# Kernel optimization log

Hardware: AMD Instinct MI355X
Metric: run time of the kernel (lower is better)

The kernel has to match this reference:

```python
import jax, jax.numpy as jnp
import numpy as np

DIM = 1536
NUM_HEADS = 24
HEAD_DIM = DIM // NUM_HEADS
SCALE = HEAD_DIM ** -0.5
B, NX, NC = 2, 2048, 256


def setup_inputs() -> dict:
    key = jax.random.key(0)
    ks = jax.random.split(key, 12)
    s = 0.02
    return {
        "x": jax.random.normal(ks[0], (B, NX, DIM), jnp.float32),
        "c": jax.random.normal(ks[1], (B, NC, DIM), jnp.float32),
        "Wqkv_x": jax.random.normal(ks[2], (3 * DIM, DIM), jnp.float32) * s,
        "bqkv_x": jax.random.normal(ks[3], (3 * DIM,), jnp.float32) * s,
        "Wqkv_c": jax.random.normal(ks[4], (3 * DIM, DIM), jnp.float32) * s,
        "bqkv_c": jax.random.normal(ks[5], (3 * DIM,), jnp.float32) * s,
        "Wproj_x": jax.random.normal(ks[6], (DIM, DIM), jnp.float32) * s,
        "bproj_x": jax.random.normal(ks[7], (DIM,), jnp.float32) * s,
        "Wproj_c": jax.random.normal(ks[8], (DIM, DIM), jnp.float32) * s,
        "bproj_c": jax.random.normal(ks[9], (DIM,), jnp.float32) * s,
    }


def _qkv(t, W, b):
    # t: [B, N, C] -> q, k, v each [B, H, N, Dh]
    Bt, N, C = t.shape
    qkv = (t @ W.T + b).reshape(Bt, N, 3, NUM_HEADS, HEAD_DIM)
    qkv = jnp.transpose(qkv, (2, 0, 3, 1, 4))  # [3, B, H, N, Dh]
    return qkv[0], qkv[1], qkv[2]


def reference(x, c, Wqkv_x, bqkv_x, Wqkv_c, bqkv_c, Wproj_x, bproj_x, Wproj_c, bproj_c):
    q_x, k_x, v_x = _qkv(x, Wqkv_x, bqkv_x)
    q_c, k_c, v_c = _qkv(c, Wqkv_c, bqkv_c)
    q = jnp.concatenate([q_x, q_c], axis=2)  # [B, H, Nx+Nc, Dh]
    k = jnp.concatenate([k_x, k_c], axis=2)
    v = jnp.concatenate([v_x, v_c], axis=2)
    attn = jnp.einsum("bhnd,bhmd->bhnm", q, k) * SCALE
    attn = jax.nn.softmax(attn, axis=-1)
    out = jnp.einsum("bhnm,bhmd->bhnd", attn, v)  # [B, H, N, Dh]
    x_out = out[:, :, :NX]
    c_out = out[:, :, NX:]
    x_out = jnp.transpose(x_out, (0, 2, 1, 3)).reshape(x.shape[0], NX, DIM)
    c_out = jnp.transpose(c_out, (0, 2, 1, 3)).reshape(c.shape[0], NC, DIM)
    return (x_out @ Wproj_x.T + bproj_x, c_out @ Wproj_c.T + bproj_c)
```

## Files before the change

kernel.cpp:

```cpp
#include <hip/hip_runtime.h>
#include <stdint.h>

#define HNUM 24
#define DIMX 1536
#define NXT  2048
#define NCT  256
#define NTOT 2304
#define BB   2

typedef __attribute__((ext_vector_type(8))) short bf16x8;
typedef __attribute__((ext_vector_type(8))) _Float16 f16x8;
typedef __attribute__((ext_vector_type(4))) _Float16 f16x4;
typedef __attribute__((ext_vector_type(2))) _Float16 f16x2;
typedef __attribute__((ext_vector_type(2))) __fp16 hp16x2;
typedef __attribute__((ext_vector_type(4))) float f32x4;
typedef __attribute__((ext_vector_type(4))) unsigned short u16x4;

#define AS1 __attribute__((address_space(1)))
#define AS3 __attribute__((address_space(3)))

__device__ __forceinline__ void glds16(const void* g, void* l) {
  __builtin_amdgcn_global_load_lds((AS1 void*)(uintptr_t)g, (AS3 void*)l, 16, 0, 0);
}

__device__ __forceinline__ unsigned short f2bf(float f) {
  unsigned int u = __float_as_uint(f);
  u += 0x7FFFu + ((u >> 16) & 1u);
  return (unsigned short)(u >> 16);
}

__device__ __forceinline__ f16x2 pkrtz(float a, float b) {
  hp16x2 r = __builtin_amdgcn_cvt_pkrtz(a, b);
  union { hp16x2 h; f16x2 f; } u;
  u.h = r;
  return u.f;
}

__device__ __forceinline__ bf16x8 ldfragB(const unsigned short* S, int row, int cc) {
  return *(const bf16x8*)(S + row * 64 + ((cc ^ (row & 7)) << 3));
}
__device__ __forceinline__ f16x4 ldVfrag(const _Float16* S, int row, int mb, int quad) {
  int gc = mb * 2 + (quad >> 1);
  int cp = gc ^ (row & 7);
  return *(const f16x4*)(S + row * 64 + cp * 8 + (quad & 1) * 4);
}

struct CastDesc { const float* src; unsigned short* dst; int start4; };
struct CastArgs { CastDesc d[6]; int total4; };

__global__ __launch_bounds__(256) void cast_all(CastArgs a) {
  int i = blockIdx.x * 256 + threadIdx.x;
  if (i >= a.total4) return;
  int r = 0;
#pragma unroll
  for (int k = 1; k < 6; ++k) r += (i >= a.d[k].start4);
  int j = i - a.d[r].start4;
  float4 v = reinterpret_cast<const float4*>(a.d[r].src)[j];
  u16x4 o;
  o[0] = f2bf(v.x); o[1] = f2bf(v.y); o[2] = f2bf(v.z); o[3] = f2bf(v.w);
  reinterpret_cast<u16x4*>(a.d[r].dst)[j] = o;
}

__device__ __forceinline__ void gemm_mainloop(
    const unsigned short* __restrict__ Ablk,
    const unsigned short* __restrict__ Wblk,
    unsigned short* As, unsigned short* Bs, f32x4 acc[4][4]) {
  const int tid  = threadIdx.x;
  const int lane = tid & 63;
  const int quad = lane >> 4, l16 = lane & 15;
  const int wave = tid >> 6;
  const int wm = (wave >> 1) * 64, wo = (wave & 1) * 64;

  for (int k0 = 0; k0 < DIMX; k0 += 64) {
    __syncthreads();
#pragma unroll
    for (int p = 0; p < 4; ++p) {
      int c = p * 256 + tid;
      int row = c >> 3;
      int kc = ((c & 7) ^ (row & 7)) << 3;
      glds16(Ablk + (size_t)row * DIMX + k0 + kc, As + c * 8);
      glds16(Wblk + (size_t)row * DIMX + k0 + kc, Bs + c * 8);
    }
    __syncthreads();
#pragma unroll
    for (int kk = 0; kk < 64; kk += 32) {
      bf16x8 af[4], bf[4];
#pragma unroll
      for (int mb = 0; mb < 4; ++mb)
        af[mb] = ldfragB(As, wm + mb * 16 + l16, (kk >> 3) + quad);
#pragma unroll
      for (int ob = 0; ob < 4; ++ob)
        bf[ob] = ldfragB(Bs, wo + ob * 16 + l16, (kk >> 3) + quad);
#pragma unroll
      for (int mb = 0; mb < 4; ++mb)
#pragma unroll
        for (int ob = 0; ob < 4; ++ob)
          acc[mb][ob] = __builtin_amdgcn_mfma_f32_16x16x32_bf16(
              af[mb], bf[ob], acc[mb][ob], 0, 0, 0);
    }
  }
}

__global__ __launch_bounds__(256, 3) void gemm_qkv(
    const unsigned short* __restrict__ xbf, const unsigned short* __restrict__ cbf,
    const unsigned short* __restrict__ Wx, const unsigned short* __restrict__ Wc,
    const float* __restrict__ bx_, const float* __restrict__ bc_,
    unsigned short* __restrict__ Qb, unsigned short* __restrict__ Kb,
    _Float16* __restrict__ VTf) {
  __shared__ unsigned short Sh[2][128 * 64];
  unsigned short* As = Sh[0];
  unsigned short* Bs = Sh[1];

  const bool isC = blockIdx.y >= 32;
  const int yloc = isC ? (int)blockIdx.y - 32 : (int)blockIdx.y;
  const int tokShift = isC ? 8 : 11;
  const int seqOff = isC ? NXT : 0;
  const unsigned short* A = (isC ? cbf : xbf) + (size_t)yloc * 128 * DIMX;
  const unsigned short* W = (isC ? Wc : Wx) + (size_t)blockIdx.x * 128 * DIMX;
  const float* bias = isC ? bc_ : bx_;

  const f32x4 z4 = {0.f, 0.f, 0.f, 0.f};
  f32x4 acc[4][4];
#pragma unroll
  for (int i = 0; i < 4; ++i)
#pragma unroll
    for (int j = 0; j < 4; ++j) acc[i][j] = z4;

  gemm_mainloop(A, W, As, Bs, acc);

  const int tid = threadIdx.x, lane = tid & 63, wave = tid >> 6;
  const int quad = lane >> 4, l16 = lane & 15;
  const int wm = (wave >> 1) * 64, wo = (wave & 1) * 64;
  const int s = blockIdx.x / 12;
  const float QSC = 0.125f * 1.44269504088896340736f;

  float bv[4];
#pragma unroll
  for (int ob = 0; ob < 4; ++ob)
    bv[ob] = bias[blockIdx.x * 128 + wo + ob * 16 + l16];

  if (s < 2) {
#pragma unroll
    for (int ob = 0; ob < 4; ++ob) {
      int o = blockIdx.x * 128 + wo + ob * 16 + l16;
      int rem = o - s * DIMX;
      int h = rem >> 6, d = rem & 63;
#pragma unroll
      for (int mb = 0; mb < 4; ++mb) {
#pragma unroll
        for (int r = 0; r < 4; ++r) {
          int m = yloc * 128 + wm + mb * 16 + quad * 4 + r;
          int b = m >> tokShift;
          int n = seqOff + (m & ((1 << tokShift) - 1));
          size_t bh = (size_t)b * HNUM + h;
          float v = acc[mb][ob][r] + bv[ob];
          if (s == 0) Qb[(bh * NTOT + n) * 64 + d] = f2bf(v * QSC);
          else        Kb[(bh * NTOT + n) * 64 + d] = f2bf(v);
        }
      }
    }
  } else {
    _Float16* Ts = (_Float16*)Sh;
    __syncthreads();
#pragma unroll
    for (int ob = 0; ob < 4; ++ob) {
      int dloc = wo + ob * 16 + l16;
      int sw = (dloc & 15) << 3;
#pragma unroll
      for (int mb = 0; mb < 4; ++mb) {
        f16x4 pk;
#pragma unroll
        for (int r = 0; r < 4; ++r) pk[r] = (_Float16)(acc[mb][ob][r] + bv[ob]);
        int m0 = wm + mb * 16 + quad * 4;
        *(f16x4*)(Ts + dloc * 128 + (m0 ^ sw)) = pk;
      }
    }
    __syncthreads();
#pragma unroll
    for (int it = 0; it < 8; ++it) {
      int cth = it * 256 + tid;
      int d = cth >> 4;
      int m0 = (cth & 15) << 3;
      f16x8 val = *(const f16x8*)(Ts + d * 128 + (m0 ^ ((d & 15) << 3)));
      int dglob = (blockIdx.x - 24) * 128 + d;
      int h = dglob >> 6, dd = dglob & 63;
      int M = yloc * 128 + m0;
      int b = M >> tokShift;
      int n = seqOff + (M & ((1 << tokShift) - 1));
      *(f16x8*)(VTf + ((size_t)(b * HNUM + h) * 64 + dd) * NTOT + n) = val;
    }
  }
}

__global__ __launch_bounds__(256, 3) void gemm_proj(
    const unsigned short* __restrict__ AX, const unsigned short* __restrict__ AC,
    const unsigned short* __restrict__ Wx, const unsigned short* __restrict__ Wc,
    const float* __restrict__ bx_, const float* __restrict__ bc_,
    float* __restrict__ out) {
  __shared__ unsigned short As[128 * 64];
  __shared__ unsigned short Bs[128 * 64];

  const bool isC = blockIdx.y >= 32;
  const int yloc = isC ? (int)blockIdx.y - 32 : (int)blockIdx.y;
  const unsigned short* A = (isC ? AC : AX) + (size_t)yloc * 128 * DIMX;
  const unsigned short* W = (isC ? Wc : Wx) + (size_t)blockIdx.x * 128 * DIMX;
  const float* bias = isC ? bc_ : bx_;
  float* o_ = out + (isC ? (size_t)BB * NXT * DIMX : (size_t)0) +
              (size_t)yloc * 128 * DIMX;

  const f32x4 z4 = {0.f, 0.f, 0.f, 0.f};
  f32x4 acc[4][4];
#pragma unroll
  for (int i = 0; i < 4; ++i)
#pragma unroll
    for (int j = 0; j < 4; ++j) acc[i][j] = z4;

  gemm_mainloop(A, W, As, Bs, acc);

  const int lane = threadIdx.x & 63, wave = threadIdx.x >> 6;
  const int quad = lane >> 4, l16 = lane & 15;
  const int wm = (wave >> 1) * 64, wo = (wave & 1) * 64;

#pragma unroll
  for (int ob = 0; ob < 4; ++ob) {
    int o = blockIdx.x * 128 + wo + ob * 16 + l16;
    float bv = bias[o];
#pragma unroll
    for (int mb = 0; mb < 4; ++mb) {
#pragma unroll
      for (int r = 0; r < 4; ++r) {
        int m = wm + mb * 16 + quad * 4 + r;
        o_[(size_t)m * DIMX + o] = acc[mb][ob][r] + bv;
      }
    }
  }
}

__global__ __launch_bounds__(512, 4) void flash_attn(
    const unsigned short* __restrict__ Qb, const unsigned short* __restrict__ Kb,
    const _Float16* __restrict__ Vf,
    unsigned short* __restrict__ AX, unsigned short* __restrict__ AC) {
  __shared__ unsigned short Ks[2][64 * 64];
  __shared__ _Float16      Vs[2][64 * 64];

  const int tid = threadIdx.x, lane = tid & 63, wave = tid >> 6;
  const int quad = lane >> 4, l16 = lane & 15;
  const int bh = blockIdx.y;
  const int qbase = blockIdx.x * 256 + wave * 32;

  bf16x8 qf[2][2];
#pragma unroll
  for (int qb = 0; qb < 2; ++qb)
#pragma unroll
    for (int kh = 0; kh < 2; ++kh)
      qf[qb][kh] = *(const bf16x8*)(
          Qb + ((size_t)bh * NTOT + qbase + qb * 16 + l16) * 64 + kh * 32 + quad * 8);

  const f32x4 z4 = {0.f, 0.f, 0.f, 0.f};
  f32x4 accT[2][4];
  float lp[2] = {0.f, 0.f};
#pragma unroll
  for (int qb = 0; qb < 2; ++qb)
#pragma unroll
    for (int db = 0; db < 4; ++db) accT[qb][db] = z4;

  const size_t kbase = (size_t)bh * NTOT * 64;
  const size_t vbase = (size_t)bh * 64 * NTOT;
  const f16x2 one2 = {(_Float16)1.f, (_Float16)1.f};

  auto stage = [&](int kt, int buf) {
    const int kv0 = kt * 64;
    int c = tid;
    int row = c >> 3;
    int kc = ((c & 7) ^ (row & 7)) << 3;
    glds16(Kb + kbase + (size_t)(kv0 + row) * 64 + kc, &Ks[buf][0] + c * 8);
    glds16(Vf + vbase + (size_t)row * NTOT + kv0 + kc, &Vs[buf][0] + c * 8);
  };

  stage(0, 0);
  for (int kt = 0; kt < 36; ++kt) {
    __syncthreads();
    if (kt < 35) stage(kt + 1, (kt + 1) & 1);
    const unsigned short* K_ = &Ks[kt & 1][0];
    const _Float16*       V_ = &Vs[kt & 1][0];

    f32x4 st[2][4];
#pragma unroll
    for (int qb = 0; qb < 2; ++qb)
#pragma unroll
      for (int mb = 0; mb < 4; ++mb) st[qb][mb] = z4;
#pragma unroll
    for (int kh = 0; kh < 2; ++kh) {
#pragma unroll
      for (int mb = 0; mb < 4; ++mb) {
        bf16x8 kf = ldfragB(K_, mb * 16 + l16, kh * 4 + quad);
#pragma unroll
        for (int qb = 0; qb < 2; ++qb)
          st[qb][mb] = __builtin_amdgcn_mfma_f32_16x16x32_bf16(
              kf, qf[qb][kh], st[qb][mb], 0, 0, 0);
      }
    }

    f16x4 pf[2][4];
#pragma unroll
    for (int qb = 0; qb < 2; ++qb)
#pragma unroll
      for (int mb = 0; mb < 4; ++mb) {
        float p0 = __builtin_amdgcn_exp2f(st[qb][mb][0]);
        float p1 = __builtin_amdgcn_exp2f(st[qb][mb][1]);
        float p2 = __builtin_amdgcn_exp2f(st[qb][mb][2]);
        float p3 = __builtin_amdgcn_exp2f(st[qb][mb][3]);
        f16x2 lo = pkrtz(p0, p1);
        f16x2 hi = pkrtz(p2, p3);
        lp[qb] = __builtin_amdgcn_fdot2(lo, one2, lp[qb], false);
        lp[qb] = __builtin_amdgcn_fdot2(hi, one2, lp[qb], false);
        f16x4 pk = {lo[0], lo[1], hi[0], hi[1]};
        pf[qb][mb] = pk;
      }

#pragma unroll
    for (int db = 0; db < 4; ++db) {
#pragma unroll
      for (int mb = 0; mb < 4; ++mb) {
        f16x4 vfr = ldVfrag(V_, db * 16 + l16, mb, quad);
#pragma unroll
        for (int qb = 0; qb < 2; ++qb)
          accT[qb][db] = __builtin_amdgcn_mfma_f32_16x16x16f16(
              vfr, pf[qb][mb], accT[qb][db], 0, 0, 0);
      }
    }
  }

  float inv[2];
#pragma unroll
  for (int qb = 0; qb < 2; ++qb) {
    float l = lp[qb];
    l += __shfl_xor(l, 16);
    l += __shfl_xor(l, 32);
    inv[qb] = __frcp_rn(l);
  }

  const int b = bh / HNUM, h = bh - b * HNUM;
#pragma unroll
  for (int qb = 0; qb < 2; ++qb) {
    int n = qbase + qb * 16 + l16;
#pragma unroll
    for (int db = 0; db < 4; ++db) {
      u16x4 o;
#pragma unroll
      for (int r = 0; r < 4; ++r) o[r] = f2bf(accT[qb][db][r] * inv[qb]);
      int col = h * 64 + db * 16 + quad * 4;
      if (n < NXT)
        *(u16x4*)(AX + ((size_t)b * NXT + n) * DIMX + col) = o;
      else
        *(u16x4*)(AC + ((size_t)b * NCT + (n - NXT)) * DIMX + col) = o;
    }
  }
}

extern "C" void kernel_launch(void* const* d_in, const int* in_sizes, int n_in,
                              void* d_out, int out_size, void* d_ws, size_t ws_size,
                              hipStream_t stream) {
  const float* x       = (const float*)d_in[0];
  const float* c       = (const float*)d_in[1];
  const float* Wqkv_x  = (const float*)d_in[2];
  const float* bqkv_x  = (const float*)d_in[3];
  const float* Wqkv_c  = (const float*)d_in[4];
  const float* bqkv_c  = (const float*)d_in[5];
  const float* Wproj_x = (const float*)d_in[6];
  const float* bproj_x = (const float*)d_in[7];
  const float* Wproj_c = (const float*)d_in[8];
  const float* bproj_c = (const float*)d_in[9];
  float* out = (float*)d_out;

  char* ws = (char*)d_ws;
  size_t off = 0;
  auto alloc = [&](size_t nelem) {
    unsigned short* p = (unsigned short*)(ws + off);
    off += nelem * 2;
    return p;
  };
  unsigned short* xbf  = alloc((size_t)BB * NXT * DIMX);
  unsigned short* cbf  = alloc((size_t)BB * NCT * DIMX);
  unsigned short* wqx  = alloc((size_t)3 * DIMX * DIMX);
  unsigned short* wqc  = alloc((size_t)3 * DIMX * DIMX);
  unsigned short* wpx  = alloc((size_t)DIMX * DIMX);
  unsigned short* wpc  = alloc((size_t)DIMX * DIMX);
  unsigned short* Qb   = alloc((size_t)BB * HNUM * NTOT * 64);
  unsigned short* Kb   = alloc((size_t)BB * HNUM * NTOT * 64);
  _Float16*       VTf  = (_Float16*)alloc((size_t)BB * HNUM * NTOT * 64);
  unsigned short* AX   = alloc((size_t)BB * NXT * DIMX);
  unsigned short* AC   = alloc((size_t)BB * NCT * DIMX);

  CastArgs ca;
  const float* srcs[6] = {x, c, Wqkv_x, Wqkv_c, Wproj_x, Wproj_c};
  unsigned short* dsts[6] = {xbf, cbf, wqx, wqc, wpx, wpc};
  size_t ns[6] = {(size_t)BB * NXT * DIMX, (size_t)BB * NCT * DIMX,
                  (size_t)3 * DIMX * DIMX, (size_t)3 * DIMX * DIMX,
                  (size_t)DIMX * DIMX, (size_t)DIMX * DIMX};
  int acc4 = 0;
  for (int i = 0; i < 6; ++i) {
    ca.d[i].src = srcs[i];
    ca.d[i].dst = dsts[i];
    ca.d[i].start4 = acc4;
    acc4 += (int)(ns[i] / 4);
  }
  ca.total4 = acc4;
  cast_all<<<dim3((acc4 + 255) / 256), dim3(256), 0, stream>>>(ca);

  gemm_qkv<<<dim3(36, 36), dim3(256), 0, stream>>>(xbf, cbf, wqx, wqc,
                                                   bqkv_x, bqkv_c, Qb, Kb, VTf);

  flash_attn<<<dim3(9, 48), dim3(512), 0, stream>>>(Qb, Kb, VTf, AX, AC);

  gemm_proj<<<dim3(12, 36), dim3(256), 0, stream>>>(AX, AC, wpx, wpc,
                                                    bproj_x, bproj_c, out);
}
```

Before: 336.9 us.

## Load V fragments directly from global into registers, drop V LDS staging

The flash attention kernel no longer stages V tiles through shared memory. Each lane now loads its V fragments straight from global memory into registers at the start of every key tile. The change also wraps the MFMA sections in s_setprio raises and relaxes the launch bound from 4 to 2 blocks per SM, giving more registers for the V fragments. This removes the LDS writes and reads for V, but the global loads are issued in the same iteration they are used, with no prefetch, so their latency may be exposed and occupancy may drop.

```diff
diff --git a/kernel.cpp b/kernel.cpp
--- a/kernel.cpp
+++ b/kernel.cpp
@@ -38,11 +38,6 @@
 
 __device__ __forceinline__ bf16x8 ldfragB(const unsigned short* S, int row, int cc) {
   return *(const bf16x8*)(S + row * 64 + ((cc ^ (row & 7)) << 3));
-}
-__device__ __forceinline__ f16x4 ldVfrag(const _Float16* S, int row, int mb, int quad) {
-  int gc = mb * 2 + (quad >> 1);
-  int cp = gc ^ (row & 7);
-  return *(const f16x4*)(S + row * 64 + cp * 8 + (quad & 1) * 4);
 }
 
 struct CastDesc { const float* src; unsigned short* dst; int start4; };
@@ -236,12 +231,11 @@
   }
 }
 
-__global__ __launch_bounds__(512, 4) void flash_attn(
+__global__ __launch_bounds__(512, 2) void flash_attn(
     const unsigned short* __restrict__ Qb, const unsigned short* __restrict__ Kb,
     const _Float16* __restrict__ Vf,
     unsigned short* __restrict__ AX, unsigned short* __restrict__ AC) {
   __shared__ unsigned short Ks[2][64 * 64];
-  __shared__ _Float16      Vs[2][64 * 64];
 
   const int tid = threadIdx.x, lane = tid & 63, wave = tid >> 6;
   const int quad = lane >> 4, l16 = lane & 15;
@@ -265,30 +259,42 @@
     for (int db = 0; db < 4; ++db) accT[qb][db] = z4;
 
   const size_t kbase = (size_t)bh * NTOT * 64;
-  const size_t vbase = (size_t)bh * 64 * NTOT;
   const f16x2 one2 = {(_Float16)1.f, (_Float16)1.f};
 
-  auto stage = [&](int kt, int buf) {
+  const _Float16* vrow[4];
+#pragma unroll
+  for (int db = 0; db < 4; ++db)
+    vrow[db] = Vf + (size_t)bh * 64 * NTOT + (size_t)(db * 16 + l16) * NTOT + quad * 4;
+
+  auto stageK = [&](int kt, int buf) {
     const int kv0 = kt * 64;
-    int c = tid;
-    int row = c >> 3;
-    int kc = ((c & 7) ^ (row & 7)) << 3;
-    glds16(Kb + kbase + (size_t)(kv0 + row) * 64 + kc, &Ks[buf][0] + c * 8);
-    glds16(Vf + vbase + (size_t)row * NTOT + kv0 + kc, &Vs[buf][0] + c * 8);
+    int row = tid >> 3;
+    int kc = ((tid & 7) ^ (row & 7)) << 3;
+    glds16(Kb + kbase + (size_t)(kv0 + row) * 64 + kc, &Ks[buf][0] + tid * 8);
   };
 
-  stage(0, 0);
+  stageK(0, 0);
   for (int kt = 0; kt < 36; ++kt) {
     __syncthreads();
-    if (kt < 35) stage(kt + 1, (kt + 1) & 1);
+
+    f16x4 VV[4][4];
+    {
+      const int kv0 = kt * 64;
+#pragma unroll
+      for (int db = 0; db < 4; ++db)
+#pragma unroll
+        for (int mb = 0; mb < 4; ++mb)
+          VV[db][mb] = *(const f16x4*)(vrow[db] + kv0 + mb * 16);
+    }
+    if (kt < 35) stageK(kt + 1, (kt + 1) & 1);
     const unsigned short* K_ = &Ks[kt & 1][0];
-    const _Float16*       V_ = &Vs[kt & 1][0];
 
     f32x4 st[2][4];
 #pragma unroll
     for (int qb = 0; qb < 2; ++qb)
 #pragma unroll
       for (int mb = 0; mb < 4; ++mb) st[qb][mb] = z4;
+    __builtin_amdgcn_s_setprio(1);
 #pragma unroll
     for (int kh = 0; kh < 2; ++kh) {
 #pragma unroll
@@ -300,6 +306,7 @@
               kf, qf[qb][kh], st[qb][mb], 0, 0, 0);
       }
     }
+    __builtin_amdgcn_s_setprio(0);
 
     f16x4 pf[2][4];
 #pragma unroll
@@ -318,17 +325,18 @@
         pf[qb][mb] = pk;
       }
 
+    __builtin_amdgcn_s_setprio(1);
 #pragma unroll
     for (int db = 0; db < 4; ++db) {
 #pragma unroll
       for (int mb = 0; mb < 4; ++mb) {
-        f16x4 vfr = ldVfrag(V_, db * 16 + l16, mb, quad);
 #pragma unroll
         for (int qb = 0; qb < 2; ++qb)
           accT[qb][db] = __builtin_amdgcn_mfma_f32_16x16x16f16(
-              vfr, pf[qb][mb], accT[qb][db], 0, 0, 0);
-      }
-    }
+              VV[db][mb], pf[qb][mb], accT[qb][db], 0, 0, 0);
+      }
+    }
+    __builtin_amdgcn_s_setprio(0);
   }
 
   float inv[2];
```

New measurement: 546.3 us. 62.2% more time.

## Software-pipeline flash attention with four-deep K/V buffering and MFMA priority

Applied to the files above, without the earlier changes.

Restructures the attention inner loop so the QK^T MFMAs for the next KV tile are issued between the exp/pack step and the PV MFMAs of the current tile. Two score accumulators alternate, and the loop is unrolled by two. K/V shared-memory buffering goes from two stages to four, so two tiles can be prefetched ahead. MFMA sections are wrapped in s_setprio raises. The aim is to hide exp latency and load latency behind matrix work. The cost is twice the LDS per block and more live registers, which will likely cut the number of resident blocks per CU.

```diff
diff --git a/kernel.cpp b/kernel.cpp
--- a/kernel.cpp
+++ b/kernel.cpp
@@ -240,8 +240,8 @@
     const unsigned short* __restrict__ Qb, const unsigned short* __restrict__ Kb,
     const _Float16* __restrict__ Vf,
     unsigned short* __restrict__ AX, unsigned short* __restrict__ AC) {
-  __shared__ unsigned short Ks[2][64 * 64];
-  __shared__ _Float16      Vs[2][64 * 64];
+  __shared__ unsigned short Ks[4][64 * 64];
+  __shared__ _Float16      Vs[4][64 * 64];
 
   const int tid = threadIdx.x, lane = tid & 63, wave = tid >> 6;
   const int quad = lane >> 4, l16 = lane & 15;
@@ -268,27 +268,22 @@
   const size_t vbase = (size_t)bh * 64 * NTOT;
   const f16x2 one2 = {(_Float16)1.f, (_Float16)1.f};
 
-  auto stage = [&](int kt, int buf) {
+  auto stageKV = [&](int kt) {
+    const int buf = kt & 3;
     const int kv0 = kt * 64;
-    int c = tid;
-    int row = c >> 3;
-    int kc = ((c & 7) ^ (row & 7)) << 3;
-    glds16(Kb + kbase + (size_t)(kv0 + row) * 64 + kc, &Ks[buf][0] + c * 8);
-    glds16(Vf + vbase + (size_t)row * NTOT + kv0 + kc, &Vs[buf][0] + c * 8);
+    int row = tid >> 3;
+    int kc = ((tid & 7) ^ (row & 7)) << 3;
+    glds16(Kb + kbase + (size_t)(kv0 + row) * 64 + kc, &Ks[buf][0] + tid * 8);
+    glds16(Vf + vbase + (size_t)row * NTOT + kv0 + kc, &Vs[buf][0] + tid * 8);
   };
 
-  stage(0, 0);
-  for (int kt = 0; kt < 36; ++kt) {
-    __syncthreads();
-    if (kt < 35) stage(kt + 1, (kt + 1) & 1);
-    const unsigned short* K_ = &Ks[kt & 1][0];
-    const _Float16*       V_ = &Vs[kt & 1][0];
-
-    f32x4 st[2][4];
+  auto qk = [&](int kt, f32x4 st[2][4]) {
 #pragma unroll
     for (int qb = 0; qb < 2; ++qb)
 #pragma unroll
       for (int mb = 0; mb < 4; ++mb) st[qb][mb] = z4;
+    const unsigned short* K_ = &Ks[kt & 3][0];
+    __builtin_amdgcn_s_setprio(1);
 #pragma unroll
     for (int kh = 0; kh < 2; ++kh) {
 #pragma unroll
@@ -300,8 +295,10 @@
               kf, qf[qb][kh], st[qb][mb], 0, 0, 0);
       }
     }
-
-    f16x4 pf[2][4];
+    __builtin_amdgcn_s_setprio(0);
+  };
+
+  auto expph = [&](f32x4 st[2][4], f16x4 pf[2][4]) {
 #pragma unroll
     for (int qb = 0; qb < 2; ++qb)
 #pragma unroll
@@ -317,7 +314,11 @@
         f16x4 pk = {lo[0], lo[1], hi[0], hi[1]};
         pf[qb][mb] = pk;
       }
-
+  };
+
+  auto pv = [&](int kt, f16x4 pf[2][4]) {
+    const _Float16* V_ = &Vs[kt & 3][0];
+    __builtin_amdgcn_s_setprio(1);
 #pragma unroll
     for (int db = 0; db < 4; ++db) {
 #pragma unroll
@@ -329,6 +330,28 @@
               vfr, pf[qb][mb], accT[qb][db], 0, 0, 0);
       }
     }
+    __builtin_amdgcn_s_setprio(0);
+  };
+
+  f32x4 stA[2][4], stB[2][4];
+  f16x4 pf[2][4];
+
+  stageKV(0);
+  stageKV(1);
+  __syncthreads();
+  qk(0, stA);
+
+  for (int kt = 0; kt < 36; kt += 2) {
+    if (kt + 2 < 36) stageKV(kt + 2);
+    expph(stA, pf);
+    qk(kt + 1, stB);
+    pv(kt, pf);
+    __syncthreads();
+    if (kt + 3 < 36) stageKV(kt + 3);
+    expph(stB, pf);
+    if (kt + 2 < 36) qk(kt + 2, stA);
+    pv(kt + 1, pf);
+    __syncthreads();
   }
 
   float inv[2];
```

Result: slower. 587.6 us (+74.4%).
